# Kernel optimization log

Measured on AMD Instinct MI355X. Metric: run time of the kernel, lower is better.

The kernel has to match this reference:

```python
import jax, jax.numpy as jnp
import numpy as np

C = 1024
HEADS = 8
HEAD_DIM = C // HEADS
SCALE = HEAD_DIM ** -0.5
GROUPS = 32
EPS = 1e-5


def _conv3(x, w, b):
    # 3x3x3 conv, padding=1 (SAME), NCDHW
    y = jax.lax.conv_general_dilated(x, w, (1, 1, 1), 'SAME',
                                     dimension_numbers=('NCDHW', 'OIDHW', 'NCDHW'))
    return y + b[None, :, None, None, None]


def _proj(x, w, b):
    # 1x1x1 conv == channel matmul; w: (C_out, C_in)
    return jnp.einsum('oc,bcdhw->bodhw', w, x) + b[None, :, None, None, None]


def _gn(x, g, b):
    B, Ch, D, H, W = x.shape
    xr = x.reshape(B, GROUPS, Ch // GROUPS, D, H, W)
    mu = xr.mean(axis=(2, 3, 4, 5), keepdims=True)
    var = xr.var(axis=(2, 3, 4, 5), keepdims=True)
    xn = ((xr - mu) * jax.lax.rsqrt(var + EPS)).reshape(B, Ch, D, H, W)
    return xn * g[None, :, None, None, None] + b[None, :, None, None, None]


def _attn(q, k, v):
    # q,k,v: (B,C,D,H,W) -> heads over channels, tokens over flattened spatial
    B, Ch, D, H, W = q.shape
    S = D * H * W
    q = q.reshape(B, HEADS, HEAD_DIM, S)
    k = k.reshape(B, HEADS, HEAD_DIM, S)
    v = v.reshape(B, HEADS, HEAD_DIM, S)
    logits = jnp.einsum('bhds,bhdt->bhst', q, k) * SCALE  # (B,H,S,S)
    a = jax.nn.softmax(logits, axis=-1)
    o = jnp.einsum('bhst,bhdt->bhds', a, v)
    return o.reshape(B, Ch, D, H, W)


def setup_inputs() -> dict:
    key = jax.random.key(0)
    ks = iter(jax.random.split(key, 40))
    def w(shape, s=0.02):
        return jax.random.normal(next(ks), shape, dtype=jnp.float32) * s
    B, D, H, W = 2, 8, 16, 16
    inp = {'x': jax.random.normal(next(ks), (B, C, D, H, W), dtype=jnp.float32)}
    for side in ('l', 'r'):
        inp[f'conv_{side}_w'] = w((C, C, 3, 3, 3))
        inp[f'conv_{side}_b'] = jnp.zeros((C,), jnp.float32)
        inp[f'gn_{side}_g'] = jnp.ones((C,), jnp.float32)
        inp[f'gn_{side}_b'] = jnp.zeros((C,), jnp.float32)
    for name in ('ql', 'kr', 'vr', 'qr', 'kl', 'vl'):
        inp[f'{name}_w'] = w((C, C))
        inp[f'{name}_b'] = jnp.zeros((C,), jnp.float32)
    inp['fus_w'] = w((C, C))
    inp['fus_b'] = jnp.zeros((C,), jnp.float32)
    inp['gn_f_g'] = jnp.ones((C,), jnp.float32)
    inp['gn_f_b'] = jnp.zeros((C,), jnp.float32)
    return inp


def reference(x, conv_l_w, conv_l_b, gn_l_g, gn_l_b,
              conv_r_w, conv_r_b, gn_r_g, gn_r_b,
              ql_w, ql_b, kr_w, kr_b, vr_w, vr_b,
              qr_w, qr_b, kl_w, kl_b, vl_w, vl_b,
              fus_w, fus_b, gn_f_g, gn_f_b):
    W = x.shape[-1]
    mid = W // 2
    x_left = x[..., :mid]
    x_right = x[..., mid:2 * mid]
    f_l = jax.nn.relu(_gn(_conv3(x_left, conv_l_w, conv_l_b), gn_l_g, gn_l_b))
    f_r = jax.nn.relu(_gn(_conv3(x_right, conv_r_w, conv_r_b), gn_r_g, gn_r_b))
    rf = jnp.flip(f_r, axis=-1)
    # left attends to flipped right
    out_l = _attn(_proj(f_l, ql_w, ql_b), _proj(rf, kr_w, kr_b), _proj(rf, vr_w, vr_b))
    # flipped right attends to left
    out_r = _attn(_proj(rf, qr_w, qr_b), _proj(f_l, kl_w, kl_b), _proj(f_l, vl_w, vl_b))
    asym_map = jnp.abs(f_l - rf).mean(axis=1, keepdims=True)
    out_r = jnp.flip(out_r, axis=-1)
    f_concat = jnp.concatenate([out_l, out_r], axis=-1)  # W even -> no pad needed
    fused = jax.nn.relu(_gn(_proj(f_concat, fus_w, fus_b), gn_f_g, gn_f_b))
    return fused, asym_map
```

## Files before the change

kernel.cpp:

```cpp
#include <hip/hip_runtime.h>
#include <hip/hip_bf16.h>
#include <stdint.h>


using bf16_t = __bf16;
using bf16x4 = __attribute__((ext_vector_type(4))) __bf16;
using bf16x8 = __attribute__((ext_vector_type(8))) __bf16;
using f32x4  = __attribute__((ext_vector_type(4))) float;

typedef const uint32_t __attribute__((address_space(1)))* gas1_t;
typedef uint32_t __attribute__((address_space(3)))* las3_t;

__device__ __forceinline__ f32x4 mfma16(bf16x8 a, bf16x8 b, f32x4 c) {
  return __builtin_amdgcn_mfma_f32_16x16x32_bf16(a, b, c, 0, 0, 0);
}
__device__ __forceinline__ void gload_lds16(const void* g, void* l) {
  __builtin_amdgcn_global_load_lds((gas1_t)g, (las3_t)l, 16, 0, 0);
}

__global__ __launch_bounds__(256) void convw_kernel(
    const float* __restrict__ wl, const float* __restrict__ wr,
    bf16_t* __restrict__ Wb)
{
  const int chunk = blockIdx.x;
// ... 2 lines not shown
  const float* __restrict__ src = (side ? wr : wl) + (size_t)co * 27648 + (size_t)chunk * 6912;
  __shared__ float L[6912];
  __shared__ bf16_t Lb[27][260];
  const int tid = threadIdx.x;
  for (int i = tid; i < 1728; i += 256)
    *(float4*)&L[i << 2] = *(const float4*)&src[i << 2];
  __syncthreads();
  {
    const int ci = tid;
#pragma unroll
    for (int t = 0; t < 27; ++t)
      Lb[t][ci] = (bf16_t)L[ci * 27 + t];
  }
  __syncthreads();
  bf16_t* __restrict__ dst = Wb + (size_t)side * (1024u * 27648u) + (size_t)co * 27648 + (chunk << 8);
  for (int u = tid; u < 864; u += 256) {
    const int t = u >> 5, c8 = (u & 31) << 3;
    const bf16x8 v = *(const bf16x8*)&Lb[t][c8];
    *(bf16x8*)&dst[(t << 10) + c8] = v;
  }
}

__global__ __launch_bounds__(256) void projw_kernel(
    const float* ql, const float* kl, const float* vl, const float* kr,
    const float* vr, const float* qr, const float* fu,
    bf16_t* __restrict__ Wp, float qs)
{
  const int z = blockIdx.y;
  const float* src; float s = 1.f;
  switch (z) {
    case 0: src = ql; s = qs; break;
    case 1: src = kl; break;
    case 2: src = vl; break;
    case 3: src = kr; break;
    case 4: src = vr; break;
    case 5: src = qr; s = qs; break;
    default: src = fu; break;
  }
  const size_t i4 = ((size_t)blockIdx.x * 256 + threadIdx.x) * 4;
  const float4 v = *(const float4*)(src + i4);
  bf16x4 o;
  o[0] = (bf16_t)(v.x * s); o[1] = (bf16_t)(v.y * s);
  o[2] = (bf16_t)(v.z * s); o[3] = (bf16_t)(v.w * s);
  *(bf16x4*)(Wp + (size_t)z * 1048576 + i4) = o;
}

__global__ __launch_bounds__(256) void xp_build_kernel(
    const float* __restrict__ x, bf16_t* __restrict__ Xp)
{
  const int cc0  = blockIdx.x << 6;
  const int d    = blockIdx.y;
  const int sb   = blockIdx.z;
  const int side = sb >> 1, b = sb & 1;
  __shared__ bf16_t Tls[64][132];
  const int tid = threadIdx.x;
#pragma unroll
  for (int j = 0; j < 8; ++j) {
    const int u = tid + (j << 8);
    const int ci = u >> 5, sub = u & 31;
// ... 3 lines not shown
    bf16x4 o;
    o[0] = (bf16_t)v.x; o[1] = (bf16_t)v.y; o[2] = (bf16_t)v.z; o[3] = (bf16_t)v.w;
    *(bf16x4*)&Tls[ci][(hh << 3) + (half << 2)] = o;
  }
  __syncthreads();
  bf16_t* __restrict__ dst = Xp + (size_t)side * 3686400 + (size_t)b * 1843200;
#pragma unroll
  for (int j = 0; j < 4; ++j) {
    const int u = tid + (j << 8);
    const int hw = u >> 3, c8 = u & 7;
    const int hh = hw >> 3, ww = hw & 7;
    bf16x8 v;
#pragma unroll
    for (int e = 0; e < 8; ++e) v[e] = Tls[(c8 << 3) + e][hw];
    *(bf16x8*)&dst[(size_t)(((d + 1) * 18 + (hh + 1)) * 10 + (ww + 1)) * 1024 + cc0 + (c8 << 3)] = v;
  }
}

__global__ __launch_bounds__(256, 4) void conv_gemm_kernel(
    const bf16_t* __restrict__ Wb, const bf16_t* __restrict__ Xp,
    bf16_t* __restrict__ Pb)
{
  const int bid = blockIdx.x;
  const int orig = ((bid & 7) << 7) | (bid >> 3);
  const int n     = orig & 15;
  const int m0    = ((orig >> 4) & 7) << 7;
  const int side  = (orig >> 7) & 1;
  const int slice = orig >> 8;
  const int t0 = slice * 7;
  const int t1 = (slice == 3) ? 27 : t0 + 7;
  const int b = n >> 3, d = n & 7;

  const bf16_t* __restrict__ A = Wb + (size_t)side * (1024u * 27648u);
  const bf16_t* __restrict__ X = Xp + (size_t)side * 3686400 + (size_t)b * 1843200;

  __shared__ bf16_t Asm[128 * 64];
  __shared__ bf16_t Bsm[128 * 64];

  const int tid = threadIdx.x;
  const int lane = tid & 63;
  const int wv = tid >> 6;
  const int wm = wv >> 1, wn = wv & 1;
  const int lane15 = lane & 15, lane4 = lane >> 4;
  const int srow0 = (wv << 5) + (lane >> 3);
  const int sc = lane & 7;

  const f32x4 fz = {0.f, 0.f, 0.f, 0.f};
  f32x4 acc[4][4];
#pragma unroll
  for (int i = 0; i < 4; ++i)
#pragma unroll
    for (int j = 0; j < 4; ++j) acc[i][j] = fz;

// ... 19 lines not shown
#pragma unroll
      for (int ks = 0; ks < 2; ++ks) {
        bf16x8 af[4];
#pragma unroll
        for (int mi = 0; mi < 4; ++mi) {
          const int row = (wm << 6) + (mi << 4) + lane15;
          const int ch = ((ks << 2) + lane4) ^ (row & 7);
          af[mi] = *(const bf16x8*)&Asm[(row << 6) + (ch << 3)];
        }
#pragma unroll
        for (int ni = 0; ni < 4; ++ni) {
          const int row = (wn << 6) + (ni << 4) + lane15;
          const int ch = ((ks << 2) + lane4) ^ (row & 7);
          const bf16x8 bfr = *(const bf16x8*)&Bsm[(row << 6) + (ch << 3)];
#pragma unroll
          for (int mi = 0; mi < 4; ++mi)
            acc[mi][ni] = mfma16(af[mi], bfr, acc[mi][ni]);
        }
      }
      __syncthreads();
    }
  }

  bf16_t* __restrict__ P = Pb + (((size_t)(slice << 1) + side) << 21);
  const int colbase = (b << 10) + (d << 7) + (wn << 6);
#pragma unroll
  for (int mi = 0; mi < 4; ++mi) {
    const int row0 = m0 + (wm << 6) + (mi << 4) + (lane4 << 2);
#pragma unroll
    for (int r = 0; r < 4; ++r) {
#pragma unroll
      for (int ni = 0; ni < 4; ++ni) {
        const int col = colbase + (ni << 4) + lane15;
        P[((size_t)(row0 + r) << 11) + col] = (bf16_t)acc[mi][ni][r];
      }
    }
  }
}

__global__ __launch_bounds__(256) void reduce4_kernel(
    const bf16_t* __restrict__ Pb, const float* __restrict__ bias_l,
    const float* __restrict__ bias_r, float* __restrict__ out_l, float* __restrict__ out_r)
{
  const int id = blockIdx.x * 256 + threadIdx.x;
  const int c8 = id & 255;
  const int co = (id >> 8) & 1023;
  const int side = id >> 18;
  const size_t off = ((size_t)co << 11) + ((size_t)c8 << 3);
  const float bia = (side ? bias_r : bias_l)[co];
  float acc[8];
#pragma unroll
  for (int e = 0; e < 8; ++e) acc[e] = bia;
#pragma unroll
  for (int s = 0; s < 4; ++s) {
    const bf16x8 v = *(const bf16x8*)&Pb[(((size_t)(s << 1) + side) << 21) + off];
#pragma unroll
    for (int e = 0; e < 8; ++e) acc[e] += (float)v[e];
  }
  float* __restrict__ outp = (side ? out_r : out_l) + off;
  float4 o0, o1;
  o0.x = acc[0]; o0.y = acc[1]; o0.z = acc[2]; o0.w = acc[3];
  o1.x = acc[4]; o1.y = acc[5]; o1.z = acc[6]; o1.w = acc[7];
  *(float4*)outp = o0;
  *(float4*)(outp + 4) = o1;
}

__device__ __forceinline__ void gemm_accum(
    const bf16_t* __restrict__ A, int lda,
    const bf16_t* __restrict__ Bt, int ldb,
    int K, f32x4 acc[4][4])
{
  __shared__ bf16_t Asm[128 * 64];
  __shared__ bf16_t Bsm[128 * 64];
  const int tid = threadIdx.x;
  const int lane = tid & 63;
  const int wv = tid >> 6;
  const int wm = wv >> 1, wn = wv & 1;
  const int lane15 = lane & 15, lane4 = lane >> 4;
  const int srow0 = (wv << 5) + (lane >> 3);
  const int sc = lane & 7;

  for (int k0 = 0; k0 < K; k0 += 64) {
#pragma unroll
    for (int i = 0; i < 4; ++i) {
      const int row = srow0 + (i << 3);
      gload_lds16(A + (size_t)row * lda + k0 + ((sc ^ (row & 7)) << 3),
                  &Asm[((wv << 2) + i) << 9]);
// ... 8 lines not shown
#pragma unroll
    for (int ks = 0; ks < 2; ++ks) {
      bf16x8 af[4];
#pragma unroll
      for (int mi = 0; mi < 4; ++mi) {
        const int row = (wm << 6) + (mi << 4) + lane15;
        const int ch = ((ks << 2) + lane4) ^ (row & 7);
        af[mi] = *(const bf16x8*)&Asm[(row << 6) + (ch << 3)];
      }
#pragma unroll
      for (int ni = 0; ni < 4; ++ni) {
        const int row = (wn << 6) + (ni << 4) + lane15;
        const int ch = ((ks << 2) + lane4) ^ (row & 7);
        const bf16x8 bfr = *(const bf16x8*)&Bsm[(row << 6) + (ch << 3)];
#pragma unroll
        for (int mi = 0; mi < 4; ++mi)
          acc[mi][ni] = mfma16(af[mi], bfr, acc[mi][ni]);
      }
    }
    __syncthreads();
  }
}

struct Proj2Args {
  const bf16_t* Bt[2];
  const float*  bias[2][3];
  float         scl[2][3];
  bf16_t*       outp[2][3];
};

__global__ __launch_bounds__(256) void proj2_kernel(const bf16_t* __restrict__ Wp, Proj2Args a)
{
  const int side = blockIdx.z;
  const int m0 = blockIdx.x << 7;
  const int n0 = blockIdx.y << 7;
  const int seg = m0 >> 10;
  const f32x4 fz = {0.f, 0.f, 0.f, 0.f};
  f32x4 acc[4][4];
#pragma unroll
  for (int i = 0; i < 4; ++i)
#pragma unroll
    for (int j = 0; j < 4; ++j) acc[i][j] = fz;
  gemm_accum(Wp + (size_t)side * 3145728 + (size_t)m0 * 1024, 1024,
             a.Bt[side] + (size_t)n0 * 1024, 1024, 1024, acc);

  const int lane = threadIdx.x & 63, wv = threadIdx.x >> 6;
  const int wm = wv >> 1, wn = wv & 1;
  const int lane15 = lane & 15, lane4 = lane >> 4;
  const float* __restrict__ bias = a.bias[side][seg];
  const float bscale = a.scl[side][seg];
  bf16_t* __restrict__ C = a.outp[side][seg];
#pragma unroll
  for (int mi = 0; mi < 4; ++mi) {
    const int rl0 = (m0 & 1023) + (wm << 6) + (mi << 4) + (lane4 << 2);
#pragma unroll
    for (int r = 0; r < 4; ++r) {
      const float bia = bias[rl0 + r] * bscale;
#pragma unroll
      for (int ni = 0; ni < 4; ++ni) {
        const int col = n0 + (wn << 6) + (ni << 4) + lane15;
        C[(size_t)(rl0 + r) * 2048 + col] = (bf16_t)(acc[mi][ni][r] + bia);
      }
    }
  }
}

__global__ __launch_bounds__(256) void fused_gemm_kernel(
    const bf16_t* __restrict__ Wf, const bf16_t* __restrict__ Bt, bf16_t* __restrict__ Pf)
{
  const int z = blockIdx.z;
  const int m0 = blockIdx.x << 7;
  const int n0 = blockIdx.y << 7;
  const f32x4 fz = {0.f, 0.f, 0.f, 0.f};
  f32x4 acc[4][4];
#pragma unroll
  for (int i = 0; i < 4; ++i)
#pragma unroll
    for (int j = 0; j < 4; ++j) acc[i][j] = fz;
  gemm_accum(Wf + (size_t)m0 * 1024 + (z << 9), 1024,
             Bt + (size_t)n0 * 1024 + (z << 9), 1024, 512, acc);

  const int lane = threadIdx.x & 63, wv = threadIdx.x >> 6;
  const int wm = wv >> 1, wn = wv & 1;
  const int lane15 = lane & 15, lane4 = lane >> 4;
  bf16_t* __restrict__ C = Pf + ((size_t)z << 22);
#pragma unroll
  for (int mi = 0; mi < 4; ++mi) {
    const int row0 = m0 + (wm << 6) + (mi << 4) + (lane4 << 2);
#pragma unroll
    for (int r = 0; r < 4; ++r) {
#pragma unroll
      for (int ni = 0; ni < 4; ++ni) {
        const int col = n0 + (wn << 6) + (ni << 4) + lane15;
        C[(size_t)(row0 + r) * 4096 + col] = (bf16_t)acc[mi][ni][r];
      }
    }
  }
}

__global__ __launch_bounds__(256) void gn_stats_lr_kernel(
    const float* __restrict__ yl, const float* __restrict__ yr,
    float* __restrict__ mu, float* __restrict__ rstd)
{
  const int id = blockIdx.x;
  const int side = id >> 6, b = (id >> 5) & 1, g = id & 31;
  const float* __restrict__ y = side ? yr : yl;
  float s = 0.f, q = 0.f;
  for (int j = threadIdx.x; j < 32768; j += 256) {
    const float v = y[(size_t)((g << 5) + (j >> 10)) * 2048 + (b << 10) + (j & 1023)];
    s += v; q += v * v;
  }
  __shared__ float sb[8];
  const int lane = threadIdx.x & 63, wv = threadIdx.x >> 6;
#pragma unroll
  for (int o = 1; o < 64; o <<= 1) { s += __shfl_xor(s, o, 64); q += __shfl_xor(q, o, 64); }
  if (lane == 0) { sb[wv] = s; sb[4 + wv] = q; }
  __syncthreads();
  if (threadIdx.x == 0) {
    const float S = sb[0] + sb[1] + sb[2] + sb[3];
    const float Q = sb[4] + sb[5] + sb[6] + sb[7];
    const float mean = S * (1.f / 32768.f);
    const float var = Q * (1.f / 32768.f) - mean * mean;
    mu[id] = mean; rstd[id] = rsqrtf(var + 1e-5f);
  }
}

__global__ __launch_bounds__(256) void gn_apply_lr_kernel(
    const float* __restrict__ yl, const float* __restrict__ yr,
    const float* __restrict__ gl, const float* __restrict__ bl,
    const float* __restrict__ gr, const float* __restrict__ br,
    const float* __restrict__ mu, const float* __restrict__ rstd,
    bf16_t* __restrict__ flT, bf16_t* __restrict__ rfT)
{
  const int side = blockIdx.z;
  const int n0 = blockIdx.x << 6;
  const int c0 = blockIdx.y << 6;
  const float* __restrict__ y = side ? yr : yl;
  const float* __restrict__ gamma = side ? gr : gl;
  const float* __restrict__ beta  = side ? br : bl;
  __shared__ float L[64][65];
  const int tid = threadIdx.x;
#pragma unroll
  for (int j = 0; j < 4; ++j) {
    const int u = tid + (j << 8);
    const int cr = u >> 4, ch = u & 15;
    const float4 v = *(const float4*)&y[(size_t)(c0 + cr) * 2048 + n0 + (ch << 2)];
    L[cr][(ch << 2) + 0] = v.x; L[cr][(ch << 2) + 1] = v.y;
    L[cr][(ch << 2) + 2] = v.z; L[cr][(ch << 2) + 3] = v.w;
  }
  __syncthreads();
  const int b = n0 >> 10;
  bf16_t* __restrict__ outT = side ? rfT : flT;
#pragma unroll
  for (int j = 0; j < 2; ++j) {
    const int u = tid + (j << 8);
    const int nr = u >> 3, c8 = u & 7;
    const int n = n0 + nr;
    const int nf = side ? ((n & ~7) | (7 - (n & 7))) : n;
    bf16x8 v;
#pragma unroll
    for (int e = 0; e < 8; ++e) {
      const int c = c0 + (c8 << 3) + e;
      const int gidx = (side << 6) + (b << 5) + (c >> 5);
      const float xv = (L[(c8 << 3) + e][nr] - mu[gidx]) * rstd[gidx] * gamma[c] + beta[c];
      v[e] = (bf16_t)fmaxf(xv, 0.f);
    }
    *(bf16x8*)&outT[(size_t)nf * 1024 + c0 + (c8 << 3)] = v;
  }
}

struct T4Args { const bf16_t* in[4]; bf16_t* out[4]; };
__global__ __launch_bounds__(256) void transpose4_kernel(T4Args a)
{
  const int z = blockIdx.z;
  const bf16_t* __restrict__ in = a.in[z];
  bf16_t* __restrict__ out = a.out[z];
  const int n0 = blockIdx.x << 6;
  const int m0 = blockIdx.y << 6;
  __shared__ bf16_t Tls[64][65];
  const int tid = threadIdx.x;
#pragma unroll
  for (int j = 0; j < 2; ++j) {
    const int u = tid + (j << 8);
    const int r = u >> 3, ch = u & 7;
    const bf16x8 v = *(const bf16x8*)&in[(size_t)(m0 + r) * 2048 + n0 + (ch << 3)];
#pragma unroll
    for (int e = 0; e < 8; ++e) Tls[r][(ch << 3) + e] = v[e];
  }
  __syncthreads();
#pragma unroll
  for (int j = 0; j < 2; ++j) {
    const int u = tid + (j << 8);
    const int rr = u >> 3, ch = u & 7;
    bf16x8 v;
#pragma unroll
    for (int e = 0; e < 8; ++e) v[e] = Tls[(ch << 3) + e][rr];
    *(bf16x8*)&out[(size_t)(n0 + rr) * 1024 + m0 + (ch << 3)] = v;
  }
}

__global__ __launch_bounds__(256, 2) void attn_kernel(
    const bf16_t* __restrict__ qlt, const bf16_t* __restrict__ krt, const bf16_t* __restrict__ vrm,
    const bf16_t* __restrict__ qrt, const bf16_t* __restrict__ klt, const bf16_t* __restrict__ vlm,
    bf16_t* __restrict__ xfc)
{
  const int st = blockIdx.x;
  const int bh = blockIdx.y;
  const int az = blockIdx.z;
  const int b = bh >> 3, h = bh & 7;
  const bf16_t* __restrict__ qt = az ? qrt : qlt;
  const bf16_t* __restrict__ kt = az ? klt : krt;
  const bf16_t* __restrict__ vm = az ? vlm : vrm;

  __shared__ bf16_t Ks[64 * 128];
  __shared__ bf16_t Vs[128 * 64];
  __shared__ bf16_t Ps[4][32 * 64];

  const int tid = threadIdx.x, lane = tid & 63, wv = tid >> 6;
  const int lane15 = lane & 15, lane4 = lane >> 4;

  bf16x8 qf[2][4];
  {
    const bf16_t* __restrict__ qbase = qt + (size_t)((b << 10) + (st << 7)) * 1024 + (h << 7);
#pragma unroll
    for (int mi = 0; mi < 2; ++mi)
#pragma unroll
      for (int kk = 0; kk < 4; ++kk) {
        const int row = (wv << 5) + (mi << 4) + lane15;
        qf[mi][kk] = *(const bf16x8*)&qbase[(size_t)row * 1024 + (kk << 5) + (lane4 << 3)];
      }
  }

  const f32x4 fz = {0.f, 0.f, 0.f, 0.f};
  f32x4 oacc[2][8];
#pragma unroll
  for (int mi = 0; mi < 2; ++mi)
#pragma unroll
    for (int nj = 0; nj < 8; ++nj) oacc[mi][nj] = fz;
  float mrun[2][4], lrun[2][4];
#pragma unroll
  for (int mi = 0; mi < 2; ++mi)
#pragma unroll
    for (int r = 0; r < 4; ++r) { mrun[mi][r] = -3.0e38f; lrun[mi][r] = 0.f; }

  for (int it = 0; it < 16; ++it) {
    __syncthreads();
#pragma unroll
    for (int j = 0; j < 4; ++j) {
      const int g = (wv << 2) + j;
      const int row = (g << 2) + lane4;
      gload_lds16(kt + (size_t)((b << 10) + (it << 6) + row) * 1024 + (h << 7) + ((lane15 ^ (row & 7)) << 3),
                  &Ks[g << 9]);
    }
#pragma unroll
    for (int j = 0; j < 4; ++j) {
      const int g = (wv << 2) + j;
      const int row = (g << 3) + (lane >> 3);
      gload_lds16(vm + (size_t)((h << 7) + row) * 2048 + (b << 10) + (it << 6) + (((lane & 7) ^ (row & 7)) << 3),
                  &Vs[g << 9]);
    }
    __syncthreads();
    f32x4 la[2][4];
#pragma unroll
    for (int mi = 0; mi < 2; ++mi)
#pragma unroll
      for (int tj = 0; tj < 4; ++tj) la[mi][tj] = fz;
#pragma unroll
    for (int kk = 0; kk < 4; ++kk) {
#pragma unroll
      for (int tj = 0; tj < 4; ++tj) {
        const int row = (tj << 4) + lane15;
        const int ch = ((kk << 2) + lane4) ^ (row & 7);
        const bf16x8 kf = *(const bf16x8*)&Ks[(row << 7) + (ch << 3)];
        la[0][tj] = mfma16(qf[0][kk], kf, la[0][tj]);
        la[1][tj] = mfma16(qf[1][kk], kf, la[1][tj]);
      }
    }
#pragma unroll
    for (int mi = 0; mi < 2; ++mi)
#pragma unroll
      for (int r = 0; r < 4; ++r) {
        float mx = la[mi][0][r];
#pragma unroll
        for (int tj = 1; tj < 4; ++tj) mx = fmaxf(mx, la[mi][tj][r]);
#pragma unroll
        for (int o = 1; o < 16; o <<= 1) mx = fmaxf(mx, __shfl_xor(mx, o, 64));
        const float mnew = fmaxf(mrun[mi][r], mx);
        const float alpha = __builtin_amdgcn_exp2f(mrun[mi][r] - mnew);
        mrun[mi][r] = mnew;
        lrun[mi][r] *= alpha;
#pragma unroll
        for (int nj = 0; nj < 8; ++nj) oacc[mi][nj][r] *= alpha;
      }
#pragma unroll
    for (int mi = 0; mi < 2; ++mi)
#pragma unroll
      for (int r = 0; r < 4; ++r) {
        const int row = (mi << 4) + (lane4 << 2) + r;
        float rs = 0.f;
#pragma unroll
        for (int tj = 0; tj < 4; ++tj) {
          const float p = __builtin_amdgcn_exp2f(la[mi][tj][r] - mrun[mi][r]);
          rs += p;
          const int byte_ = ((tj << 5) + (lane15 << 1)) ^ ((row & 7) << 4);
          *(bf16_t*)((char*)(&Ps[wv][0]) + (row << 7) + byte_) = (bf16_t)p;
        }
#pragma unroll
        for (int o = 1; o < 16; o <<= 1) rs += __shfl_xor(rs, o, 64);
        lrun[mi][r] += rs;
      }
#pragma unroll
    for (int kk = 0; kk < 2; ++kk) {
      bf16x8 pf[2];
#pragma unroll
      for (int mi = 0; mi < 2; ++mi) {
        const int row = (mi << 4) + lane15;
        const int ch = ((kk << 2) + lane4) ^ (row & 7);
        pf[mi] = *(const bf16x8*)&Ps[wv][(row << 6) + (ch << 3)];
      }
#pragma unroll
      for (int nj = 0; nj < 8; ++nj) {
        const int row = (nj << 4) + lane15;
        const int ch = ((kk << 2) + lane4) ^ (row & 7);
        const bf16x8 vf = *(const bf16x8*)&Vs[(row << 6) + (ch << 3)];
        oacc[0][nj] = mfma16(pf[0], vf, oacc[0][nj]);
        oacc[1][nj] = mfma16(pf[1], vf, oacc[1][nj]);
      }
    }
  }
#pragma unroll
  for (int mi = 0; mi < 2; ++mi)
#pragma unroll
    for (int r = 0; r < 4; ++r) {
      const int sl = (wv << 5) + (mi << 4) + (lane4 << 2) + r;
      const int s = (st << 7) + sl;
      const int dd = s >> 7, hh2 = (s >> 3) & 15, ww = s & 7;
      const int w16 = az ? (15 - ww) : ww;
      const int n16 = (b << 11) + ((dd << 4) + hh2) * 16 + w16;
      const float inv = 1.f / lrun[mi][r];
#pragma unroll
      for (int nj = 0; nj < 8; ++nj) {
        const int c = (h << 7) + (nj << 4) + lane15;
        xfc[(size_t)n16 * 1024 + c] = (bf16_t)(oacc[mi][nj][r] * inv);
      }
    }
}

__global__ __launch_bounds__(256) void gn_partial_f_kernel(
    const bf16_t* __restrict__ Pf, const float* __restrict__ bias,
    float* __restrict__ pS, float* __restrict__ pQ)
{
  const int bg = blockIdx.x;
  const int sl = blockIdx.y;
  const int b = bg >> 5, g = bg & 31;
  const int tid = threadIdx.x;
  const int c = (g << 5) + (tid >> 3);
  const int s0 = (sl << 8) + ((tid & 7) << 5);
  const size_t base = (size_t)c * 4096 + (b << 11) + s0;
  const float bia = bias[c];
  float s = 0.f, q = 0.f;
#pragma unroll
  for (int u = 0; u < 4; ++u) {
    const bf16x8 v0 = *(const bf16x8*)&Pf[base + (u << 3)];
    const bf16x8 v1 = *(const bf16x8*)&Pf[base + (u << 3) + 4194304];
#pragma unroll
    for (int e = 0; e < 8; ++e) {
      const float v = (float)v0[e] + (float)v1[e] + bia;
      s += v; q += v * v;
    }
  }
  __shared__ float sb[8];
  const int lane = tid & 63, wv = tid >> 6;
#pragma unroll
  for (int o = 1; o < 64; o <<= 1) { s += __shfl_xor(s, o, 64); q += __shfl_xor(q, o, 64); }
  if (lane == 0) { sb[wv] = s; sb[4 + wv] = q; }
  __syncthreads();
  if (tid == 0) {
    pS[(bg << 3) + sl] = sb[0] + sb[1] + sb[2] + sb[3];
    pQ[(bg << 3) + sl] = sb[4] + sb[5] + sb[6] + sb[7];
  }
}

__global__ __launch_bounds__(64) void gn_final_f_kernel(
    const float* __restrict__ pS, const float* __restrict__ pQ,
    float* __restrict__ mu, float* __restrict__ rstd)
{
  const int bg = threadIdx.x;
  float S = 0.f, Q = 0.f;
#pragma unroll
  for (int sl = 0; sl < 8; ++sl) { S += pS[(bg << 3) + sl]; Q += pQ[(bg << 3) + sl]; }
  const float mean = S * (1.f / 65536.f);
  const float var = Q * (1.f / 65536.f) - mean * mean;
  mu[bg] = mean; rstd[bg] = rsqrtf(var + 1e-5f);
}

__global__ __launch_bounds__(256) void gn_apply_f_kernel(
    const bf16_t* __restrict__ Pf, const float* __restrict__ bias,
    const float* __restrict__ gamma, const float* __restrict__ beta,
    const float* __restrict__ mu, const float* __restrict__ rstd,
    float* __restrict__ outp)
{
  const int id = blockIdx.x * 256 + threadIdx.x;
  const int s8 = id & 255;
  const int c = (id >> 8) & 1023;
  const int b = id >> 18;
  const int gidx = (b << 5) + (c >> 5);
  const float m = mu[gidx], rs = rstd[gidx], gm = gamma[c], bt = beta[c], bia = bias[c];
  const size_t idx = (size_t)c * 4096 + (b << 11) + (s8 << 3);
  const bf16x8 v0 = *(const bf16x8*)&Pf[idx];
  const bf16x8 v1 = *(const bf16x8*)&Pf[idx + 4194304];
  float o[8];
#pragma unroll
  for (int e = 0; e < 8; ++e) {
    const float v = (float)v0[e] + (float)v1[e] + bia;
    o[e] = fmaxf((v - m) * rs * gm + bt, 0.f);
  }
  float* __restrict__ op = &outp[(((size_t)(b << 10) + c) << 11) + (s8 << 3)];
  float4 o0, o1;
  o0.x = o[0]; o0.y = o[1]; o0.z = o[2]; o0.w = o[3];
  o1.x = o[4]; o1.y = o[5]; o1.z = o[6]; o1.w = o[7];
  *(float4*)op = o0;
  *(float4*)(op + 4) = o1;
}

__global__ __launch_bounds__(256) void asym_kernel(
    const bf16_t* __restrict__ flT, const bf16_t* __restrict__ rfT, float* __restrict__ outp)
{
  const int n = blockIdx.x;
  const int tid = threadIdx.x;
  const bf16x4 a = *(const bf16x4*)&flT[(size_t)n * 1024 + (tid << 2)];
// ... 22 lines not shown
  const float* glb_ = (const float*)d_in[4];
  const float* crw  = (const float*)d_in[5];
  const float* crb  = (const float*)d_in[6];
  const float* grg  = (const float*)d_in[7];
  const float* grb  = (const float*)d_in[8];
  const float* qlw = (const float*)d_in[9];  const float* qlb = (const float*)d_in[10];
  const float* krw = (const float*)d_in[11]; const float* krb = (const float*)d_in[12];
  const float* vrw = (const float*)d_in[13]; const float* vrb = (const float*)d_in[14];
  const float* qrw = (const float*)d_in[15]; const float* qrb = (const float*)d_in[16];
  const float* klw = (const float*)d_in[17]; const float* klb = (const float*)d_in[18];
  const float* vlw = (const float*)d_in[19]; const float* vlb = (const float*)d_in[20];
  const float* fuw = (const float*)d_in[21]; const float* fub = (const float*)d_in[22];
  const float* gfg = (const float*)d_in[23]; const float* gfb = (const float*)d_in[24];
  float* out = (float*)d_out;

  char* ws = (char*)d_ws;
  size_t off = 0;
  auto take = [&](size_t bytes) -> char* {
    char* p = ws + off; off += (bytes + 255) & ~(size_t)255; return p;
  };
  bf16_t* Wb    = (bf16_t*)take(113246208ull);
  bf16_t* Wp    = (bf16_t*)take(14680064ull);
  bf16_t* Xp    = (bf16_t*)take(14745600ull);
  float*  convL = (float*) take(8388608ull);
  float*  convR = (float*) take(8388608ull);
  bf16_t* flT   = (bf16_t*)take(4194304ull);
  bf16_t* rfT   = (bf16_t*)take(4194304ull);
  float*  gmu   = (float*) take(512);
  float*  grs   = (float*) take(512);
  float*  gfmu  = (float*) take(256);
  float*  gfrs  = (float*) take(256);
  float*  pS    = (float*) take(2048);
  float*  pQ    = (float*) take(2048);
  bf16_t* Pb    = (bf16_t*)take(33554432ull);

  char* al = (char*)Wb; size_t aoff = 0;
  auto takeA = [&](size_t bytes) -> char* {
    char* p = al + aoff; aoff += (bytes + 255) & ~(size_t)255; return p;
  };
  bf16_t* qlR = (bf16_t*)takeA(4194304ull);
  bf16_t* krR = (bf16_t*)takeA(4194304ull);
  bf16_t* qrR = (bf16_t*)takeA(4194304ull);
  bf16_t* klR = (bf16_t*)takeA(4194304ull);
  bf16_t* Vr  = (bf16_t*)takeA(4194304ull);
  bf16_t* Vl  = (bf16_t*)takeA(4194304ull);
  bf16_t* qlT = (bf16_t*)takeA(4194304ull);
  bf16_t* krT = (bf16_t*)takeA(4194304ull);
  bf16_t* qrT = (bf16_t*)takeA(4194304ull);
  bf16_t* klT = (bf16_t*)takeA(4194304ull);
  bf16_t* xfcT = (bf16_t*)takeA(8388608ull);
  bf16_t* Pf   = (bf16_t*)takeA(16777216ull);

  const float QS = 0.08838834764831843f * 1.4426950408889634f;

  hipMemsetAsync(Xp, 0, 14745600ull, stream);
  convw_kernel<<<dim3(4, 1024, 2), 256, 0, stream>>>(clw, crw, Wb);
  projw_kernel<<<dim3(1024, 7), 256, 0, stream>>>(qlw, klw, vlw, krw, vrw, qrw, fuw, Wp, QS);
  xp_build_kernel<<<dim3(16, 8, 4), 256, 0, stream>>>(x, Xp);
  conv_gemm_kernel<<<dim3(1024), 256, 0, stream>>>(Wb, Xp, Pb);
  reduce4_kernel<<<dim3(2048), 256, 0, stream>>>(Pb, clb, crb, convL, convR);
  gn_stats_lr_kernel<<<dim3(128), 256, 0, stream>>>(convL, convR, gmu, grs);
  gn_apply_lr_kernel<<<dim3(32, 16, 2), 256, 0, stream>>>(convL, convR, glg, glb_, grg, grb,
                                                          gmu, grs, flT, rfT);
  Proj2Args pa;
  pa.Bt[0] = flT; pa.Bt[1] = rfT;
  pa.bias[0][0] = qlb; pa.bias[0][1] = klb; pa.bias[0][2] = vlb;
  pa.bias[1][0] = krb; pa.bias[1][1] = vrb; pa.bias[1][2] = qrb;
  pa.scl[0][0] = QS;  pa.scl[0][1] = 1.f; pa.scl[0][2] = 1.f;
  pa.scl[1][0] = 1.f; pa.scl[1][1] = 1.f; pa.scl[1][2] = QS;
  pa.outp[0][0] = qlR; pa.outp[0][1] = klR; pa.outp[0][2] = Vl;
  pa.outp[1][0] = krR; pa.outp[1][1] = Vr;  pa.outp[1][2] = qrR;
  proj2_kernel<<<dim3(24, 16, 2), 256, 0, stream>>>(Wp, pa);

  T4Args ta;
  ta.in[0] = qlR; ta.in[1] = krR; ta.in[2] = qrR; ta.in[3] = klR;
  ta.out[0] = qlT; ta.out[1] = krT; ta.out[2] = qrT; ta.out[3] = klT;
  transpose4_kernel<<<dim3(32, 16, 4), 256, 0, stream>>>(ta);

  attn_kernel<<<dim3(8, 16, 2), 256, 0, stream>>>(qlT, krT, Vr, qrT, klT, Vl, xfcT);
  fused_gemm_kernel<<<dim3(8, 32, 2), 256, 0, stream>>>(Wp + 6ull * 1048576, xfcT, Pf);
  gn_partial_f_kernel<<<dim3(64, 8), 256, 0, stream>>>(Pf, fub, pS, pQ);
  gn_final_f_kernel<<<dim3(1), 64, 0, stream>>>(pS, pQ, gfmu, gfrs);
  gn_apply_f_kernel<<<dim3(2048), 256, 0, stream>>>(Pf, fub, gfg, gfb, gfmu, gfrs, out);
  asym_kernel<<<dim3(2048), 256, 0, stream>>>(flT, rfT, out + 4194304);
}
```

Measured before the change: 493.6 us.

## Restructure conv split-K, fuse GN stats, drop transposes, shrink attention tiles

Raises conv split-K from 4 to 5 slices to give 1280 blocks, and folds the left/right GroupNorm statistics into the reduction kernel through atomics. The Q/K projections now write their transposed layout directly, so the transpose kernel goes away, and V gets its own projection kernel. Attention moves to 64-query tiles (16 rows per wave, twice as many blocks) and skips the rescale when the running max grows by 8 or less. The final GN finalize kernel is merged into the apply kernel. This removes several launches and intermediate passes, at the cost of more partial-sum traffic and float atomics whose summation order varies between runs.

```diff
diff --git a/kernel.cpp b/kernel.cpp
--- a/kernel.cpp
+++ b/kernel.cpp
@@ -48,8 +48,8 @@
 }
 
 __global__ __launch_bounds__(256) void projw_kernel(
-    const float* ql, const float* kl, const float* vl, const float* kr,
-    const float* vr, const float* qr, const float* fu,
+    const float* ql, const float* kl, const float* kr, const float* qr,
+    const float* vl, const float* vr, const float* fu,
     bf16_t* __restrict__ Wp, float qs)
 {
   const int z = blockIdx.y;
@@ -57,10 +57,10 @@
   switch (z) {
     case 0: src = ql; s = qs; break;
     case 1: src = kl; break;
-    case 2: src = vl; break;
-    case 3: src = kr; break;
-    case 4: src = vr; break;
-    case 5: src = qr; s = qs; break;
+    case 2: src = kr; break;
+    case 3: src = qr; s = qs; break;
+    case 4: src = vl; break;
+    case 5: src = vr; break;
     default: src = fu; break;
   }
   const size_t i4 = ((size_t)blockIdx.x * 256 + threadIdx.x) * 4;
@@ -110,13 +110,14 @@
     bf16_t* __restrict__ Pb)
 {
   const int bid = blockIdx.x;
-  const int orig = ((bid & 7) << 7) | (bid >> 3);
+  const int orig = (bid & 7) * 160 + (bid >> 3);
   const int n     = orig & 15;
   const int m0    = ((orig >> 4) & 7) << 7;
   const int side  = (orig >> 7) & 1;
   const int slice = orig >> 8;
-  const int t0 = slice * 7;
-  const int t1 = (slice == 3) ? 27 : t0 + 7;
+  const int T0[5] = {0, 6, 12, 17, 22};
+  const int T1[5] = {6, 12, 17, 22, 27};
+  const int t0 = T0[slice], t1 = T1[slice];
   const int b = n >> 3, d = n & 7;
 
   const bf16_t* __restrict__ A = Wb + (size_t)side * (1024u * 27648u);
@@ -182,7 +183,7 @@
     }
   }
 
-  bf16_t* __restrict__ P = Pb + (((size_t)(slice << 1) + side) << 21);
+  bf16_t* __restrict__ P = Pb + (((size_t)slice * 2 + side) << 21);
   const int colbase = (b << 10) + (d << 7) + (wn << 6);
 #pragma unroll
   for (int mi = 0; mi < 4; ++mi) {
@@ -198,11 +199,13 @@
   }
 }
 
-__global__ __launch_bounds__(256) void reduce4_kernel(
+__global__ __launch_bounds__(256) void reduce5_kernel(
     const bf16_t* __restrict__ Pb, const float* __restrict__ bias_l,
-    const float* __restrict__ bias_r, float* __restrict__ out_l, float* __restrict__ out_r)
+    const float* __restrict__ bias_r, float* __restrict__ out_l, float* __restrict__ out_r,
+    float* __restrict__ pS_lr, float* __restrict__ pQ_lr)
 {
   const int id = blockIdx.x * 256 + threadIdx.x;
+  const int tid = threadIdx.x;
   const int c8 = id & 255;
   const int co = (id >> 8) & 1023;
   const int side = id >> 18;
@@ -212,8 +215,8 @@
 #pragma unroll
   for (int e = 0; e < 8; ++e) acc[e] = bia;
 #pragma unroll
-  for (int s = 0; s < 4; ++s) {
-    const bf16x8 v = *(const bf16x8*)&Pb[(((size_t)(s << 1) + side) << 21) + off];
+  for (int s = 0; s < 5; ++s) {
+    const bf16x8 v = *(const bf16x8*)&Pb[(((size_t)s * 2 + side) << 21) + off];
 #pragma unroll
     for (int e = 0; e < 8; ++e) acc[e] += (float)v[e];
   }
@@ -223,6 +226,22 @@
   o1.x = acc[4]; o1.y = acc[5]; o1.z = acc[6]; o1.w = acc[7];
   *(float4*)outp = o0;
   *(float4*)(outp + 4) = o1;
+  float s = 0.f, q = 0.f;
+#pragma unroll
+  for (int e = 0; e < 8; ++e) { s += acc[e]; q += acc[e] * acc[e]; }
+  __shared__ float sb[8];
+  const int lane = tid & 63, wv = tid >> 6;
+#pragma unroll
+  for (int o = 1; o < 64; o <<= 1) { s += __shfl_xor(s, o, 64); q += __shfl_xor(q, o, 64); }
+  if (lane == 0) { sb[wv] = s; sb[4 + wv] = q; }
+  __syncthreads();
+  if (tid == 0) {
+    const int g = (side << 6) + (co >> 5);
+    atomicAdd(&pS_lr[g],      sb[0] + sb[1]);
+    atomicAdd(&pS_lr[g + 32], sb[2] + sb[3]);
+    atomicAdd(&pQ_lr[g],      sb[4] + sb[5]);
+    atomicAdd(&pQ_lr[g + 32], sb[6] + sb[7]);
+  }
 }
 
 __device__ __forceinline__ void gemm_accum(
@@ -277,18 +296,17 @@
   }
 }
 
-struct Proj2Args {
-  const bf16_t* Bt[2];
-  const float*  bias[2][3];
-  float         scl[2][3];
-  bf16_t*       outp[2][3];
+struct ProjTArgs {
+  const bf16_t* act[2];
+  const float*  bias[2][2];
+  float         scl[2][2];
+  bf16_t*       outp[2][2];
 };
-
-__global__ __launch_bounds__(256) void proj2_kernel(const bf16_t* __restrict__ Wp, Proj2Args a)
+__global__ __launch_bounds__(256) void proj_t_kernel(const bf16_t* __restrict__ Wp, ProjTArgs a)
 {
   const int side = blockIdx.z;
-  const int m0 = blockIdx.x << 7;
-  const int n0 = blockIdx.y << 7;
+  const int n0 = blockIdx.x << 7;
+  const int m0 = blockIdx.y << 7;
   const int seg = m0 >> 10;
   const f32x4 fz = {0.f, 0.f, 0.f, 0.f};
   f32x4 acc[4][4];
@@ -296,8 +314,8 @@
   for (int i = 0; i < 4; ++i)
 #pragma unroll
     for (int j = 0; j < 4; ++j) acc[i][j] = fz;
-  gemm_accum(Wp + (size_t)side * 3145728 + (size_t)m0 * 1024, 1024,
-             a.Bt[side] + (size_t)n0 * 1024, 1024, 1024, acc);
+  gemm_accum(a.act[side] + (size_t)n0 * 1024, 1024,
+             Wp + (size_t)side * 2097152 + (size_t)m0 * 1024, 1024, 1024, acc);
 
   const int lane = threadIdx.x & 63, wv = threadIdx.x >> 6;
   const int wm = wv >> 1, wn = wv & 1;
@@ -305,16 +323,56 @@
   const float* __restrict__ bias = a.bias[side][seg];
   const float bscale = a.scl[side][seg];
   bf16_t* __restrict__ C = a.outp[side][seg];
+  const int mloc = (m0 & 1023) + (wn << 6);
+  float bv[4];
+#pragma unroll
+  for (int ni = 0; ni < 4; ++ni) bv[ni] = bias[mloc + (ni << 4) + lane15] * bscale;
 #pragma unroll
   for (int mi = 0; mi < 4; ++mi) {
-    const int rl0 = (m0 & 1023) + (wm << 6) + (mi << 4) + (lane4 << 2);
+    const int rowb = n0 + (wm << 6) + (mi << 4) + (lane4 << 2);
 #pragma unroll
     for (int r = 0; r < 4; ++r) {
-      const float bia = bias[rl0 + r] * bscale;
+#pragma unroll
+      for (int ni = 0; ni < 4; ++ni) {
+        const int col = mloc + (ni << 4) + lane15;
+        C[(size_t)(rowb + r) * 1024 + col] = (bf16_t)(acc[mi][ni][r] + bv[ni]);
+      }
+    }
+  }
+}
+
+__global__ __launch_bounds__(256) void proj_v_kernel(
+    const bf16_t* __restrict__ Wp, const bf16_t* __restrict__ flT,
+    const bf16_t* __restrict__ rfT, const float* __restrict__ vlb,
+    const float* __restrict__ vrb, bf16_t* __restrict__ Vl, bf16_t* __restrict__ Vr)
+{
+  const int side = blockIdx.z;
+  const int m0 = blockIdx.x << 7;
+  const int n0 = blockIdx.y << 7;
+  const f32x4 fz = {0.f, 0.f, 0.f, 0.f};
+  f32x4 acc[4][4];
+#pragma unroll
+  for (int i = 0; i < 4; ++i)
+#pragma unroll
+    for (int j = 0; j < 4; ++j) acc[i][j] = fz;
+  gemm_accum(Wp + 4194304ull + (size_t)side * 1048576 + (size_t)m0 * 1024, 1024,
+             (side ? rfT : flT) + (size_t)n0 * 1024, 1024, 1024, acc);
+
+  const int lane = threadIdx.x & 63, wv = threadIdx.x >> 6;
+  const int wm = wv >> 1, wn = wv & 1;
+  const int lane15 = lane & 15, lane4 = lane >> 4;
+  const float* __restrict__ bias = side ? vrb : vlb;
+  bf16_t* __restrict__ C = side ? Vr : Vl;
+#pragma unroll
+  for (int mi = 0; mi < 4; ++mi) {
+    const int row0 = m0 + (wm << 6) + (mi << 4) + (lane4 << 2);
+#pragma unroll
+    for (int r = 0; r < 4; ++r) {
+      const float bia = bias[row0 + r];
 #pragma unroll
       for (int ni = 0; ni < 4; ++ni) {
         const int col = n0 + (wn << 6) + (ni << 4) + lane15;
-        C[(size_t)(rl0 + r) * 2048 + col] = (bf16_t)(acc[mi][ni][r] + bia);
+        C[(size_t)(row0 + r) * 2048 + col] = (bf16_t)(acc[mi][ni][r] + bia);
       }
     }
   }
@@ -353,38 +411,11 @@
   }
 }
 
-__global__ __launch_bounds__(256) void gn_stats_lr_kernel(
-    const float* __restrict__ yl, const float* __restrict__ yr,
-    float* __restrict__ mu, float* __restrict__ rstd)
-{
-  const int id = blockIdx.x;
-  const int side = id >> 6, b = (id >> 5) & 1, g = id & 31;
-  const float* __restrict__ y = side ? yr : yl;
-  float s = 0.f, q = 0.f;
-  for (int j = threadIdx.x; j < 32768; j += 256) {
-    const float v = y[(size_t)((g << 5) + (j >> 10)) * 2048 + (b << 10) + (j & 1023)];
-    s += v; q += v * v;
-  }
-  __shared__ float sb[8];
-  const int lane = threadIdx.x & 63, wv = threadIdx.x >> 6;
-#pragma unroll
-  for (int o = 1; o < 64; o <<= 1) { s += __shfl_xor(s, o, 64); q += __shfl_xor(q, o, 64); }
-  if (lane == 0) { sb[wv] = s; sb[4 + wv] = q; }
-  __syncthreads();
-  if (threadIdx.x == 0) {
-    const float S = sb[0] + sb[1] + sb[2] + sb[3];
-    const float Q = sb[4] + sb[5] + sb[6] + sb[7];
-    const float mean = S * (1.f / 32768.f);
-    const float var = Q * (1.f / 32768.f) - mean * mean;
-    mu[id] = mean; rstd[id] = rsqrtf(var + 1e-5f);
-  }
-}
-
 __global__ __launch_bounds__(256) void gn_apply_lr_kernel(
     const float* __restrict__ yl, const float* __restrict__ yr,
     const float* __restrict__ gl, const float* __restrict__ bl,
     const float* __restrict__ gr, const float* __restrict__ br,
-    const float* __restrict__ mu, const float* __restrict__ rstd,
+    const float* __restrict__ pS_lr, const float* __restrict__ pQ_lr,
     bf16_t* __restrict__ flT, bf16_t* __restrict__ rfT)
 {
   const int side = blockIdx.z;
@@ -412,45 +443,18 @@
     const int nr = u >> 3, c8 = u & 7;
     const int n = n0 + nr;
     const int nf = side ? ((n & ~7) | (7 - (n & 7))) : n;
+    const int cbase = c0 + (c8 << 3);
+    const int gidx = (side << 6) + (b << 5) + (cbase >> 5);
+    const float m = pS_lr[gidx] * (1.f / 32768.f);
+    const float rs = rsqrtf(pQ_lr[gidx] * (1.f / 32768.f) - m * m + 1e-5f);
     bf16x8 v;
 #pragma unroll
     for (int e = 0; e < 8; ++e) {
-      const int c = c0 + (c8 << 3) + e;
-      const int gidx = (side << 6) + (b << 5) + (c >> 5);
-      const float xv = (L[(c8 << 3) + e][nr] - mu[gidx]) * rstd[gidx] * gamma[c] + beta[c];
+      const int c = cbase + e;
+      const float xv = (L[(c8 << 3) + e][nr] - m) * rs * gamma[c] + beta[c];
       v[e] = (bf16_t)fmaxf(xv, 0.f);
     }
-    *(bf16x8*)&outT[(size_t)nf * 1024 + c0 + (c8 << 3)] = v;
-  }
-}
-
-struct T4Args { const bf16_t* in[4]; bf16_t* out[4]; };
-__global__ __launch_bounds__(256) void transpose4_kernel(T4Args a)
-{
-  const int z = blockIdx.z;
-  const bf16_t* __restrict__ in = a.in[z];
-  bf16_t* __restrict__ out = a.out[z];
-  const int n0 = blockIdx.x << 6;
-  const int m0 = blockIdx.y << 6;
-  __shared__ bf16_t Tls[64][65];
-  const int tid = threadIdx.x;
-#pragma unroll
-  for (int j = 0; j < 2; ++j) {
-    const int u = tid + (j << 8);
-    const int r = u >> 3, ch = u & 7;
-    const bf16x8 v = *(const bf16x8*)&in[(size_t)(m0 + r) * 2048 + n0 + (ch << 3)];
-#pragma unroll
-    for (int e = 0; e < 8; ++e) Tls[r][(ch << 3) + e] = v[e];
-  }
-  __syncthreads();
-#pragma unroll
-  for (int j = 0; j < 2; ++j) {
-    const int u = tid + (j << 8);
-    const int rr = u >> 3, ch = u & 7;
-    bf16x8 v;
-#pragma unroll
-    for (int e = 0; e < 8; ++e) v[e] = Tls[(ch << 3) + e][rr];
-    *(bf16x8*)&out[(size_t)(n0 + rr) * 1024 + m0 + (ch << 3)] = v;
+    *(bf16x8*)&outT[(size_t)nf * 1024 + cbase] = v;
   }
 }
 
@@ -469,34 +473,27 @@
 
   __shared__ bf16_t Ks[64 * 128];
   __shared__ bf16_t Vs[128 * 64];
-  __shared__ bf16_t Ps[4][32 * 64];
+  __shared__ bf16_t Ps[4][16 * 64];
 
   const int tid = threadIdx.x, lane = tid & 63, wv = tid >> 6;
   const int lane15 = lane & 15, lane4 = lane >> 4;
 
-  bf16x8 qf[2][4];
+  bf16x8 qf[4];
   {
-    const bf16_t* __restrict__ qbase = qt + (size_t)((b << 10) + (st << 7)) * 1024 + (h << 7);
-#pragma unroll
-    for (int mi = 0; mi < 2; ++mi)
-#pragma unroll
-      for (int kk = 0; kk < 4; ++kk) {
-        const int row = (wv << 5) + (mi << 4) + lane15;
-        qf[mi][kk] = *(const bf16x8*)&qbase[(size_t)row * 1024 + (kk << 5) + (lane4 << 3)];
-      }
+    const bf16_t* __restrict__ qbase = qt + (size_t)((b << 10) + (st << 6)) * 1024 + (h << 7);
+    const int row = (wv << 4) + lane15;
+#pragma unroll
+    for (int kk = 0; kk < 4; ++kk)
+      qf[kk] = *(const bf16x8*)&qbase[(size_t)row * 1024 + (kk << 5) + (lane4 << 3)];
   }
 
   const f32x4 fz = {0.f, 0.f, 0.f, 0.f};
-  f32x4 oacc[2][8];
-#pragma unroll
-  for (int mi = 0; mi < 2; ++mi)
-#pragma unroll
-    for (int nj = 0; nj < 8; ++nj) oacc[mi][nj] = fz;
-  float mrun[2][4], lrun[2][4];
-#pragma unroll
-  for (int mi = 0; mi < 2; ++mi)
-#pragma unroll
-    for (int r = 0; r < 4; ++r) { mrun[mi][r] = -3.0e38f; lrun[mi][r] = 0.f; }
+  f32x4 oacc[8];
+#pragma unroll
+  for (int nj = 0; nj < 8; ++nj) oacc[nj] = fz;
+  float mrun[4], lrun[4];
+#pragma unroll
+  for (int r = 0; r < 4; ++r) { mrun[r] = -3.0e38f; lrun[r] = 0.f; }
 
   for (int it = 0; it < 16; ++it) {
     __syncthreads();
@@ -515,11 +512,9 @@
                   &Vs[g << 9]);
     }
     __syncthreads();
-    f32x4 la[2][4];
-#pragma unroll
-    for (int mi = 0; mi < 2; ++mi)
-#pragma unroll
-      for (int tj = 0; tj < 4; ++tj) la[mi][tj] = fz;
+    f32x4 la[4];
+#pragma unroll
+    for (int tj = 0; tj < 4; ++tj) la[tj] = fz;
 #pragma unroll
     for (int kk = 0; kk < 4; ++kk) {
 #pragma unroll
@@ -527,78 +522,75 @@
         const int row = (tj << 4) + lane15;
         const int ch = ((kk << 2) + lane4) ^ (row & 7);
         const bf16x8 kf = *(const bf16x8*)&Ks[(row << 7) + (ch << 3)];
-        la[0][tj] = mfma16(qf[0][kk], kf, la[0][tj]);
-        la[1][tj] = mfma16(qf[1][kk], kf, la[1][tj]);
-      }
-    }
-#pragma unroll
-    for (int mi = 0; mi < 2; ++mi)
+        la[tj] = mfma16(qf[kk], kf, la[tj]);
+      }
+    }
+    float mx[4];
+    int ok = 1;
+#pragma unroll
+    for (int r = 0; r < 4; ++r) {
+      float m_ = la[0][r];
+#pragma unroll
+      for (int tj = 1; tj < 4; ++tj) m_ = fmaxf(m_, la[tj][r]);
+#pragma unroll
+      for (int o = 1; o < 16; o <<= 1) m_ = fmaxf(m_, __shfl_xor(m_, o, 64));
+      mx[r] = m_;
+      ok &= (m_ <= mrun[r] + 8.f) ? 1 : 0;
+    }
+    if (!__all(ok)) {
 #pragma unroll
       for (int r = 0; r < 4; ++r) {
-        float mx = la[mi][0][r];
-#pragma unroll
-        for (int tj = 1; tj < 4; ++tj) mx = fmaxf(mx, la[mi][tj][r]);
-#pragma unroll
-        for (int o = 1; o < 16; o <<= 1) mx = fmaxf(mx, __shfl_xor(mx, o, 64));
-        const float mnew = fmaxf(mrun[mi][r], mx);
-        const float alpha = __builtin_amdgcn_exp2f(mrun[mi][r] - mnew);
-        mrun[mi][r] = mnew;
-        lrun[mi][r] *= alpha;
-#pragma unroll
-        for (int nj = 0; nj < 8; ++nj) oacc[mi][nj][r] *= alpha;
-      }
-#pragma unroll
-    for (int mi = 0; mi < 2; ++mi)
-#pragma unroll
-      for (int r = 0; r < 4; ++r) {
-        const int row = (mi << 4) + (lane4 << 2) + r;
-        float rs = 0.f;
-#pragma unroll
-        for (int tj = 0; tj < 4; ++tj) {
-          const float p = __builtin_amdgcn_exp2f(la[mi][tj][r] - mrun[mi][r]);
-          rs += p;
-          const int byte_ = ((tj << 5) + (lane15 << 1)) ^ ((row & 7) << 4);
-          *(bf16_t*)((char*)(&Ps[wv][0]) + (row << 7) + byte_) = (bf16_t)p;
-        }
-#pragma unroll
-        for (int o = 1; o < 16; o <<= 1) rs += __shfl_xor(rs, o, 64);
-        lrun[mi][r] += rs;
-      }
+        const float mnew = fmaxf(mrun[r], mx[r]);
+        const float alpha = __builtin_amdgcn_exp2f(mrun[r] - mnew);
+        mrun[r] = mnew;
+        lrun[r] *= alpha;
+#pragma unroll
+        for (int nj = 0; nj < 8; ++nj) oacc[nj][r] *= alpha;
+      }
+    }
+#pragma unroll
+    for (int r = 0; r < 4; ++r) {
+      const int row = (lane4 << 2) + r;
+      float rs = 0.f;
+#pragma unroll
+      for (int tj = 0; tj < 4; ++tj) {
+        const float p = __builtin_amdgcn_exp2f(la[tj][r] - mrun[r]);
+        rs += p;
+        const int byte_ = ((tj << 5) + (lane15 << 1)) ^ ((row & 7) << 4);
+        *(bf16_t*)((char*)(&Ps[wv][0]) + (row << 7) + byte_) = (bf16_t)p;
+      }
+#pragma unroll
+      for (int o = 1; o < 16; o <<= 1) rs += __shfl_xor(rs, o, 64);
+      lrun[r] += rs;
+    }
 #pragma unroll
     for (int kk = 0; kk < 2; ++kk) {
-      bf16x8 pf[2];
-#pragma unroll
-      for (int mi = 0; mi < 2; ++mi) {
-        const int row = (mi << 4) + lane15;
-        const int ch = ((kk << 2) + lane4) ^ (row & 7);
-        pf[mi] = *(const bf16x8*)&Ps[wv][(row << 6) + (ch << 3)];
-      }
+      const int prow = lane15;
+      const int pch = ((kk << 2) + lane4) ^ (prow & 7);
+      const bf16x8 pf = *(const bf16x8*)&Ps[wv][(prow << 6) + (pch << 3)];
 #pragma unroll
       for (int nj = 0; nj < 8; ++nj) {
         const int row = (nj << 4) + lane15;
         const int ch = ((kk << 2) + lane4) ^ (row & 7);
         const bf16x8 vf = *(const bf16x8*)&Vs[(row << 6) + (ch << 3)];
-        oacc[0][nj] = mfma16(pf[0], vf, oacc[0][nj]);
-        oacc[1][nj] = mfma16(pf[1], vf, oacc[1][nj]);
-      }
-    }
-  }
-#pragma unroll
-  for (int mi = 0; mi < 2; ++mi)
-#pragma unroll
-    for (int r = 0; r < 4; ++r) {
-      const int sl = (wv << 5) + (mi << 4) + (lane4 << 2) + r;
-      const int s = (st << 7) + sl;
-      const int dd = s >> 7, hh2 = (s >> 3) & 15, ww = s & 7;
-      const int w16 = az ? (15 - ww) : ww;
-      const int n16 = (b << 11) + ((dd << 4) + hh2) * 16 + w16;
-      const float inv = 1.f / lrun[mi][r];
-#pragma unroll
-      for (int nj = 0; nj < 8; ++nj) {
-        const int c = (h << 7) + (nj << 4) + lane15;
-        xfc[(size_t)n16 * 1024 + c] = (bf16_t)(oacc[mi][nj][r] * inv);
-      }
-    }
+        oacc[nj] = mfma16(pf, vf, oacc[nj]);
+      }
+    }
+  }
+#pragma unroll
+  for (int r = 0; r < 4; ++r) {
+    const int sl = (wv << 4) + (lane4 << 2) + r;
+    const int s = (st << 6) + sl;
+    const int dd = s >> 7, hh2 = (s >> 3) & 15, ww = s & 7;
+    const int w16 = az ? (15 - ww) : ww;
+    const int n16 = (b << 11) + ((dd << 4) + hh2) * 16 + w16;
+    const float inv = 1.f / lrun[r];
+#pragma unroll
+    for (int nj = 0; nj < 8; ++nj) {
+      const int c = (h << 7) + (nj << 4) + lane15;
+      xfc[(size_t)n16 * 1024 + c] = (bf16_t)(oacc[nj][r] * inv);
+    }
+  }
 }
 
 __global__ __launch_bounds__(256) void gn_partial_f_kernel(
@@ -636,23 +628,10 @@
   }
 }
 
-__global__ __launch_bounds__(64) void gn_final_f_kernel(
-    const float* __restrict__ pS, const float* __restrict__ pQ,
-    float* __restrict__ mu, float* __restrict__ rstd)
-{
-  const int bg = threadIdx.x;
-  float S = 0.f, Q = 0.f;
-#pragma unroll
-  for (int sl = 0; sl < 8; ++sl) { S += pS[(bg << 3) + sl]; Q += pQ[(bg << 3) + sl]; }
-  const float mean = S * (1.f / 65536.f);
-  const float var = Q * (1.f / 65536.f) - mean * mean;
-  mu[bg] = mean; rstd[bg] = rsqrtf(var + 1e-5f);
-}
-
 __global__ __launch_bounds__(256) void gn_apply_f_kernel(
     const bf16_t* __restrict__ Pf, const float* __restrict__ bias,
     const float* __restrict__ gamma, const float* __restrict__ beta,
-    const float* __restrict__ mu, const float* __restrict__ rstd,
+    const float* __restrict__ pS, const float* __restrict__ pQ,
     float* __restrict__ outp)
 {
   const int id = blockIdx.x * 256 + threadIdx.x;
@@ -660,7 +639,12 @@
   const int c = (id >> 8) & 1023;
   const int b = id >> 18;
   const int gidx = (b << 5) + (c >> 5);
-  const float m = mu[gidx], rs = rstd[gidx], gm = gamma[c], bt = beta[c], bia = bias[c];
+  float S = 0.f, Q = 0.f;
+#pragma unroll
+  for (int sl = 0; sl < 8; ++sl) { S += pS[(gidx << 3) + sl]; Q += pQ[(gidx << 3) + sl]; }
+  const float m = S * (1.f / 65536.f);
+  const float rs = rsqrtf(Q * (1.f / 65536.f) - m * m + 1e-5f);
+  const float gm = gamma[c], bt = beta[c], bia = bias[c];
   const size_t idx = (size_t)c * 4096 + (b << 11) + (s8 << 3);
   const bf16x8 v0 = *(const bf16x8*)&Pf[idx];
   const bf16x8 v1 = *(const bf16x8*)&Pf[idx + 4194304];
@@ -729,65 +713,53 @@
   bf16_t* Wb    = (bf16_t*)take(113246208ull);
   bf16_t* Wp    = (bf16_t*)take(14680064ull);
   bf16_t* Xp    = (bf16_t*)take(14745600ull);
+  float*  pS_lr = (float*) take(512);
+  float*  pQ_lr = (float*) take(512);
   float*  convL = (float*) take(8388608ull);
   float*  convR = (float*) take(8388608ull);
   bf16_t* flT   = (bf16_t*)take(4194304ull);
   bf16_t* rfT   = (bf16_t*)take(4194304ull);
-  float*  gmu   = (float*) take(512);
-  float*  grs   = (float*) take(512);
-  float*  gfmu  = (float*) take(256);
-  float*  gfrs  = (float*) take(256);
   float*  pS    = (float*) take(2048);
   float*  pQ    = (float*) take(2048);
-  bf16_t* Pb    = (bf16_t*)take(33554432ull);
+  bf16_t* Pb    = (bf16_t*)take(41943040ull);
 
   char* al = (char*)Wb; size_t aoff = 0;
   auto takeA = [&](size_t bytes) -> char* {
     char* p = al + aoff; aoff += (bytes + 255) & ~(size_t)255; return p;
   };
-  bf16_t* qlR = (bf16_t*)takeA(4194304ull);
-  bf16_t* krR = (bf16_t*)takeA(4194304ull);
-  bf16_t* qrR = (bf16_t*)takeA(4194304ull);
-  bf16_t* klR = (bf16_t*)takeA(4194304ull);
-  bf16_t* Vr  = (bf16_t*)takeA(4194304ull);
-  bf16_t* Vl  = (bf16_t*)takeA(4194304ull);
   bf16_t* qlT = (bf16_t*)takeA(4194304ull);
+  bf16_t* klT = (bf16_t*)takeA(4194304ull);
   bf16_t* krT = (bf16_t*)takeA(4194304ull);
   bf16_t* qrT = (bf16_t*)takeA(4194304ull);
-  bf16_t* klT = (bf16_t*)takeA(4194304ull);
+  bf16_t* Vl  = (bf16_t*)takeA(4194304ull);
+  bf16_t* Vr  = (bf16_t*)takeA(4194304ull);
   bf16_t* xfcT = (bf16_t*)takeA(8388608ull);
   bf16_t* Pf   = (bf16_t*)takeA(16777216ull);
 
   const float QS = 0.08838834764831843f * 1.4426950408889634f;
 
-  hipMemsetAsync(Xp, 0, 14745600ull, stream);
+  hipMemsetAsync(Xp, 0, 14745600ull + 1024ull, stream);
   convw_kernel<<<dim3(4, 1024, 2), 256, 0, stream>>>(clw, crw, Wb);
-  projw_kernel<<<dim3(1024, 7), 256, 0, stream>>>(qlw, klw, vlw, krw, vrw, qrw, fuw, Wp, QS);
+  projw_kernel<<<dim3(1024, 7), 256, 0, stream>>>(qlw, klw, krw, qrw, vlw, vrw, fuw, Wp, QS);
   xp_build_kernel<<<dim3(16, 8, 4), 256, 0, stream>>>(x, Xp);
-  conv_gemm_kernel<<<dim3(1024), 256, 0, stream>>>(Wb, Xp, Pb);
-  reduce4_kernel<<<dim3(2048), 256, 0, stream>>>(Pb, clb, crb, convL, convR);
-  gn_stats_lr_kernel<<<dim3(128), 256, 0, stream>>>(convL, convR, gmu, grs);
+  conv_gemm_kernel<<<dim3(1280), 256, 0, stream>>>(Wb, Xp, Pb);
+  reduce5_kernel<<<dim3(2048), 256, 0, stream>>>(Pb, clb, crb, convL, convR, pS_lr, pQ_lr);
   gn_apply_lr_kernel<<<dim3(32, 16, 2), 256, 0, stream>>>(convL, convR, glg, glb_, grg, grb,
-                                                          gmu, grs, flT, rfT);
-  Proj2Args pa;
-  pa.Bt[0] = flT; pa.Bt[1] = rfT;
-  pa.bias[0][0] = qlb; pa.bias[0][1] = klb; pa.bias[0][2] = vlb;
-  pa.bias[1][0] = krb; pa.bias[1][1] = vrb; pa.bias[1][2] = qrb;
-  pa.scl[0][0] = QS;  pa.scl[0][1] = 1.f; pa.scl[0][2] = 1.f;
-  pa.scl[1][0] = 1.f; pa.scl[1][1] = 1.f; pa.scl[1][2] = QS;
-  pa.outp[0][0] = qlR; pa.outp[0][1] = klR; pa.outp[0][2] = Vl;
-  pa.outp[1][0] = krR; pa.outp[1][1] = Vr;  pa.outp[1][2] = qrR;
-  proj2_kernel<<<dim3(24, 16, 2), 256, 0, stream>>>(Wp, pa);
-
-  T4Args ta;
-  ta.in[0] = qlR; ta.in[1] = krR; ta.in[2] = qrR; ta.in[3] = klR;
-  ta.out[0] = qlT; ta.out[1] = krT; ta.out[2] = qrT; ta.out[3] = klT;
-  transpose4_kernel<<<dim3(32, 16, 4), 256, 0, stream>>>(ta);
-
-  attn_kernel<<<dim3(8, 16, 2), 256, 0, stream>>>(qlT, krT, Vr, qrT, klT, Vl, xfcT);
+                                                          pS_lr, pQ_lr, flT, rfT);
+  ProjTArgs pa;
+  pa.act[0] = flT; pa.act[1] = rfT;
+  pa.bias[0][0] = qlb; pa.bias[0][1] = klb;
+  pa.bias[1][0] = krb; pa.bias[1][1] = qrb;
+  pa.scl[0][0] = QS;  pa.scl[0][1] = 1.f;
+  pa.scl[1][0] = 1.f; pa.scl[1][1] = QS;
+  pa.outp[0][0] = qlT; pa.outp[0][1] = klT;
+  pa.outp[1][0] = krT; pa.outp[1][1] = qrT;
+  proj_t_kernel<<<dim3(16, 16, 2), 256, 0, stream>>>(Wp, pa);
+  proj_v_kernel<<<dim3(8, 16, 2), 256, 0, stream>>>(Wp, flT, rfT, vlb, vrb, Vl, Vr);
+
+  attn_kernel<<<dim3(16, 16, 2), 256, 0, stream>>>(qlT, krT, Vr, qrT, klT, Vl, xfcT);
   fused_gemm_kernel<<<dim3(8, 32, 2), 256, 0, stream>>>(Wp + 6ull * 1048576, xfcT, Pf);
   gn_partial_f_kernel<<<dim3(64, 8), 256, 0, stream>>>(Pf, fub, pS, pQ);
-  gn_final_f_kernel<<<dim3(1), 64, 0, stream>>>(pS, pQ, gfmu, gfrs);
-  gn_apply_f_kernel<<<dim3(2048), 256, 0, stream>>>(Pf, fub, gfg, gfb, gfmu, gfrs, out);
+  gn_apply_f_kernel<<<dim3(2048), 256, 0, stream>>>(Pf, fub, gfg, gfb, pS, pQ, out);
   asym_kernel<<<dim3(2048), 256, 0, stream>>>(flT, rfT, out + 4194304);
 }
```

New measurement: 515.7 us. +4.5%, slower.
